# Optimization experiments

Measured on AMD Instinct MI355X. Metric: run time of the kernel, lower is better.

## Reference

```python
import jax, jax.numpy as jnp
import numpy as np

N = 4096      # tokens per modality
DIM = 514     # input feature dim
OUT = 256     # out_dim (per-head width, head=1)
NC = 2        # num_classes
LN_EPS = 1e-5


def setup_inputs() -> dict:
    key = jax.random.key(0)
    ks = jax.random.split(key, 12)
    def nrm(k, shape, s=0.02):
        return jax.random.normal(k, shape, dtype=jnp.float32) * s
    return {
        "t1": jax.random.normal(ks[0], (N, DIM), dtype=jnp.float32),
        "t2": jax.random.normal(ks[1], (N, DIM), dtype=jnp.float32),
        "t1c": jax.random.normal(ks[2], (N, DIM), dtype=jnp.float32),
        "Wqkv1": nrm(ks[3], (DIM, 3 * OUT)), "bqkv1": jnp.zeros((3 * OUT,), jnp.float32),
        "Wqkv2": nrm(ks[4], (DIM, 3 * OUT)), "bqkv2": jnp.zeros((3 * OUT,), jnp.float32),
        "Wqkv3": nrm(ks[5], (DIM, 3 * OUT)), "bqkv3": jnp.zeros((3 * OUT,), jnp.float32),
        "Wo1": nrm(ks[6], (2 * OUT, DIM)), "bo1": jnp.zeros((DIM,), jnp.float32),
        "Wo2": nrm(ks[7], (2 * OUT, DIM)), "bo2": jnp.zeros((DIM,), jnp.float32),
        "Wo3": nrm(ks[8], (2 * OUT, DIM)), "bo3": jnp.zeros((DIM,), jnp.float32),
        "ln_g": jnp.ones((3 * DIM,), jnp.float32),
        "ln_b": jnp.zeros((3 * DIM,), jnp.float32),
        "Wh": nrm(ks[9], (3 * DIM, NC)), "bh": jnp.zeros((NC,), jnp.float32),
    }


def _forward(t1, t2, t1c, Wqkv1, bqkv1, Wqkv2, bqkv2, Wqkv3, bqkv3,
             Wo1, bo1, Wo2, bo2, Wo3, bo3, ln_g, ln_b, Wh, bh):
    # QKV projections (head=1 so no head reshape needed)
    q1, k1, v1 = jnp.split(t1 @ Wqkv1 + bqkv1, 3, axis=-1)   # each [n, OUT]
    q2, k2, v2 = jnp.split(t2 @ Wqkv2 + bqkv2, 3, axis=-1)
    q3, k3, v3 = jnp.split(t1c @ Wqkv3 + bqkv3, 3, axis=-1)

    # Six cross-attention instances batched into one group dim g=6.
    # Order: out12, out13, out21, out23, out31, out32  (q_x attends to k_y/v_y)
    qs = jnp.stack([q2, q3, q1, q3, q1, q2])                  # [6, n, OUT]
    ks_ = jnp.stack([k1, k1, k2, k2, k3, k3])
    vs = jnp.stack([v1, v1, v2, v2, v3, v3])
    # NOTE: original code applies NO 1/sqrt(d) scale
    attn = jax.nn.softmax(jnp.einsum('gid,gjd->gij', qs, ks_), axis=-1)
    outs = jnp.einsum('gij,gjd->gid', attn, vs)               # [6, n, OUT]
    out12, out13, out21, out23, out31, out32 = outs

    # residual add with duplicated keys, then per-modality output proj + residual
    t1r = jnp.concatenate([out21, out31], -1) + jnp.concatenate([k1, k1], -1)
    t2r = jnp.concatenate([out12, out32], -1) + jnp.concatenate([k2, k2], -1)
    t3r = jnp.concatenate([out13, out23], -1) + jnp.concatenate([k3, k3], -1)
    a1 = t1r @ Wo1 + bo1 + t1                                 # [n, DIM]
    a2 = t2r @ Wo2 + bo2 + t2
    a3 = t3r @ Wo3 + bo3 + t1c

    atten = jnp.concatenate([a1, a2, a3], -1)                 # [n, 3*DIM]
    mu = jnp.mean(atten, axis=-1, keepdims=True)
    var = jnp.var(atten, axis=-1, keepdims=True)
    normed = (atten - mu) * jax.lax.rsqrt(var + LN_EPS) * ln_g + ln_b
    out = normed @ Wh + bh                                    # [n, NC]
    feat = atten[None]                                        # [1, n, 3*DIM]
    return out, feat


def reference(t1, t2, t1c, Wqkv1, bqkv1, Wqkv2, bqkv2, Wqkv3, bqkv3,
              Wo1, bo1, Wo2, bo2, Wo3, bo3, ln_g, ln_b, Wh, bh):
    return _forward(t1, t2, t1c, Wqkv1, bqkv1, Wqkv2, bqkv2, Wqkv3, bqkv3,
                    Wo1, bo1, Wo2, bo2, Wo3, bo3, ln_g, ln_b, Wh, bh)
```

## Files before the change

### kernel.cpp

```cpp
#include <hip/hip_runtime.h>
#include <hip/hip_bf16.h>

typedef unsigned short u16;
typedef unsigned int u32;
typedef __attribute__((ext_vector_type(8))) __bf16 bf16x8;
typedef __attribute__((ext_vector_type(4))) float f32x4;
typedef __attribute__((ext_vector_type(16))) float f32x16;

#define N_TOK 4096
#define DIMF  514
#define KPAD  544
#define OUT3  768
#define OUTD  256
#define RDIM  512
#define DIMP  640
#define FDIM  1542
#define SHIFT 16.0f
#define NCHUNK 4
#define KTILES ((N_TOK / NCHUNK) / 32)

__device__ __forceinline__ bf16x8 ld_frag(const u16* p) {
    return __builtin_bit_cast(bf16x8, *reinterpret_cast<const uint4*>(p));
}
__device__ __forceinline__ u16 f2bf(float x) {
    return __builtin_bit_cast(u16, __float2bfloat16(x));
}
__device__ __forceinline__ float bf2f(u16 u) {
    return __bfloat162float(__builtin_bit_cast(__hip_bfloat16, u));
}
__device__ __forceinline__ f32x16 mfma_b(bf16x8 a, bf16x8 b, f32x16 c) {
    return __builtin_amdgcn_mfma_f32_32x32x16_bf16(a, b, c, 0, 0, 0);
}
__device__ __forceinline__ f32x4 mfma16(bf16x8 a, bf16x8 b, f32x4 c) {
    return __builtin_amdgcn_mfma_f32_16x16x32_bf16(a, b, c, 0, 0, 0);
}
__device__ __forceinline__ void gl_lds16(const u16* g, u16* l) {
    __builtin_amdgcn_global_load_lds(
        (const __attribute__((address_space(1))) void*)(g),
        (__attribute__((address_space(3))) void*)(l), 16, 0, 0);
}

__global__ void prep_kernel(const float* __restrict__ t1, const float* __restrict__ t2,
                            const float* __restrict__ t1c,
                            const float* __restrict__ W1, const float* __restrict__ W2,
                            const float* __restrict__ W3,
                            const float* __restrict__ Wo1, const float* __restrict__ Wo2,
                            const float* __restrict__ Wo3,
                            u16* __restrict__ tA, u16* __restrict__ WqkvT,
                            u16* __restrict__ WoT)
{
    int idx = blockIdx.x * blockDim.x + threadIdx.x;
    const int TA_N = 3 * N_TOK * KPAD;
    const int WQ_N = 3 * OUT3 * KPAD;
    const int WO_N = 3 * DIMP * RDIM;
    if (idx < TA_N) {
        int m = idx / (N_TOK * KPAD);
        int rem = idx - m * (N_TOK * KPAD);
        int row = rem / KPAD;
        int col = rem - row * KPAD;
        const float* t = (m == 0) ? t1 : (m == 1) ? t2 : t1c;
        tA[idx] = (col < DIMF) ? f2bf(t[row * DIMF + col]) : (u16)0;
    } else if (idx < TA_N + WQ_N) {
        int i = idx - TA_N;
        int m = i / (OUT3 * KPAD);
        int rem = i - m * (OUT3 * KPAD);
        int n = rem / KPAD;
        int c = rem - n * KPAD;
        const float* W = (m == 0) ? W1 : (m == 1) ? W2 : W3;
        WqkvT[i] = (c < DIMF) ? f2bf(W[c * OUT3 + n]) : (u16)0;
    } else if (idx < TA_N + WQ_N + WO_N) {
        int i = idx - TA_N - WQ_N;
        int m = i / (DIMP * RDIM);
        int rem = i - m * (DIMP * RDIM);
        int n = rem / RDIM;
        int c = rem - n * RDIM;
        const float* W = (m == 0) ? Wo1 : (m == 1) ? Wo2 : Wo3;
        WoT[i] = (n < DIMF) ? f2bf(W[c * DIMF + n]) : (u16)0;
    }
}

__global__ __launch_bounds__(256, 2) void qkv_gemm(
    const u16* __restrict__ tA, const u16* __restrict__ WqkvT,
    const float* __restrict__ b1, const float* __restrict__ b2, const float* __restrict__ b3,
    u16* __restrict__ qbuf, u16* __restrict__ kbuf, u16* __restrict__ vT)
{
    const int mt = blockIdx.x, nt = blockIdx.y, mod = blockIdx.z;
    const u16* A = tA + mod * (N_TOK * KPAD);
    const u16* B = WqkvT + mod * (OUT3 * KPAD);
    const float* bias = (mod == 0) ? b1 : (mod == 1) ? b2 : b3;

    __shared__ alignas(16) u16 Fbuf[2][16 * 512];

    const int tid = threadIdx.x;
    const int lane = tid & 63;
    const int w = tid >> 6;
    const int wm = w & 1, wn = w >> 1;
    const int l31 = lane & 31, h = lane >> 5;

    auto stage = [&](int kt, u16* dst) {
#pragma unroll
        for (int fi = 0; fi < 4; fi++) {
            int f = w * 4 + fi;
            int rb = (f & 7) >> 1, kc = f & 1;
            const u16* src = (f < 8)
                ? &A[(mt * 128 + rb * 32 + l31) * KPAD + kt * 32 + kc * 16 + h * 8]
                : &B[(nt * 128 + rb * 32 + l31) * KPAD + kt * 32 + kc * 16 + h * 8];
            gl_lds16(src, dst + f * 512);
        }
    };

    f32x16 acc[2][2];
#pragma unroll
    for (int i = 0; i < 2; i++)
#pragma unroll
        for (int j = 0; j < 2; j++)
#pragma unroll
            for (int r = 0; r < 16; r++) acc[i][j][r] = 0.f;

    stage(0, Fbuf[0]);
    __syncthreads();

    for (int kt = 0; kt < KPAD / 32; kt++) {
        const int p = kt & 1;
        if (kt + 1 < KPAD / 32) stage(kt + 1, Fbuf[p ^ 1]);
        const u16* FB = Fbuf[p];
#pragma unroll
        for (int kc = 0; kc < 2; kc++) {
            bf16x8 af[2], bfr[2];
#pragma unroll
            for (int mr = 0; mr < 2; mr++)
                af[mr] = ld_frag(&FB[((wm * 2 + mr) * 2 + kc) * 512 + lane * 8]);
#pragma unroll
            for (int nr = 0; nr < 2; nr++)
                bfr[nr] = ld_frag(&FB[(8 + (wn * 2 + nr) * 2 + kc) * 512 + lane * 8]);
#pragma unroll
            for (int mr = 0; mr < 2; mr++)
#pragma unroll
                for (int nr = 0; nr < 2; nr++)
                    acc[mr][nr] = mfma_b(af[mr], bfr[nr], acc[mr][nr]);
        }
        __syncthreads();
    }

    u16* qb = qbuf + mod * (N_TOK * OUTD);
    u16* kb = kbuf + mod * (N_TOK * OUTD);
    u16* vb = vT + mod * (OUTD * N_TOK);
#pragma unroll
    for (int mr = 0; mr < 2; mr++)
#pragma unroll
        for (int nr = 0; nr < 2; nr++)
#pragma unroll
            for (int r = 0; r < 16; r++) {
                int row = mt * 128 + wm * 64 + mr * 32 + (r & 3) + 8 * (r >> 2) + 4 * h;
                int col = nt * 128 + wn * 64 + nr * 32 + l31;
                u16 bv = f2bf(acc[mr][nr][r] + bias[col]);
                int cs = col >> 8, cc = col & 255;
                if (cs == 0)      qb[row * OUTD + cc] = bv;
                else if (cs == 1) kb[row * OUTD + cc] = bv;
                else              vb[cc * N_TOK + row] = bv;
            }
}

__global__ __launch_bounds__(256, 2) void attn_kernel(
    const u16* __restrict__ qbuf, const u16* __restrict__ kbuf,
    const u16* __restrict__ vT, u16* __restrict__ Opart, float* __restrict__ lpart)
{
    const int qt = blockIdx.x;
    const int g  = blockIdx.y;
    const int c  = blockIdx.z;
    const int kv = g >> 1;
    const int mn = (kv == 0) ? 1 : 0;
    const int mx = (kv == 2) ? 1 : 2;
    const int qm = (g & 1) ? mx : mn;

    const u16* Qg = qbuf + qm * (N_TOK * OUTD);
    const u16* Kg = kbuf + kv * (N_TOK * OUTD);
    const u16* Vg = vT + kv * (OUTD * N_TOK);
    u16* Op = Opart + ((size_t)(c * 6 + g) * N_TOK + qt * 128) * OUTD;
    float* lp = lpart + (c * 6 + g) * N_TOK + qt * 128;

    __shared__ alignas(16) u16 Fbuf[2][32 * 512];

    const int tid = threadIdx.x;
    const int lane = tid & 63;
    const int w = tid >> 6;
    const int l31 = lane & 31, h = lane >> 5;
    const int sl = lane & 15, sg = lane >> 4;
    const int q0 = qt * 128 + w * 32;

    auto stage = [&](int k0, u16* dst) {
        if (w < 2) {
#pragma unroll
            for (int fi = 0; fi < 8; fi++) {
                gl_lds16(&Kg[(k0 + w * 16 + sl) * OUTD + fi * 32 + sg * 8],
                         dst + (w * 8 + fi) * 512);
            }
        } else {
#pragma unroll
            for (int fi = 0; fi < 8; fi++) {
                int f = (w - 2) * 8 + fi;
                int nb = f >> 1, half = f & 1;
                gl_lds16(&Vg[(nb * 32 + l31) * N_TOK + k0 + half * 16 + h * 8],
                         dst + (16 + f) * 512);
            }
        }
    };

    const int k0base = c * (N_TOK / NCHUNK);

    stage(k0base, Fbuf[0]);

    bf16x8 qf[16];
#pragma unroll
    for (int j = 0; j < 8; j++)
#pragma unroll
        for (int qh = 0; qh < 2; qh++)
            qf[2 * j + qh] = ld_frag(&Qg[(q0 + qh * 16 + sl) * OUTD + j * 32 + sg * 8]);

    f32x16 Oacc[8];
#pragma unroll
    for (int nb = 0; nb < 8; nb++)
#pragma unroll
        for (int r = 0; r < 16; r++) Oacc[nb][r] = 0.f;
    float lsA0 = 0.f, lsA1 = 0.f;

    __syncthreads();

    for (int kt = 0; kt < KTILES; kt++) {
        const int p = kt & 1;
        if (kt + 1 < KTILES) stage(k0base + (kt + 1) * 32, Fbuf[p ^ 1]);
        const u16* FB = Fbuf[p];

        f32x4 Sq[2][2];
#pragma unroll
        for (int a = 0; a < 2; a++)
#pragma unroll
            for (int b = 0; b < 2; b++)
#pragma unroll
                for (int r = 0; r < 4; r++) Sq[a][b][r] = 0.f;
        __builtin_amdgcn_s_setprio(1);
#pragma unroll
        for (int j = 0; j < 8; j++) {
            bf16x8 kf0 = ld_frag(&FB[j * 512 + lane * 8]);
            bf16x8 kf1 = ld_frag(&FB[(8 + j) * 512 + lane * 8]);
            Sq[0][0] = mfma16(kf0, qf[2 * j], Sq[0][0]);
            Sq[0][1] = mfma16(kf0, qf[2 * j + 1], Sq[0][1]);
            Sq[1][0] = mfma16(kf1, qf[2 * j], Sq[1][0]);
            Sq[1][1] = mfma16(kf1, qf[2 * j + 1], Sq[1][1]);
        }
        __builtin_amdgcn_s_setprio(0);

        u32 pk[2][2][2];
#pragma unroll
        for (int kh = 0; kh < 2; kh++)
#pragma unroll
            for (int qh = 0; qh < 2; qh++) {
                float e0 = __expf(Sq[kh][qh][0] - SHIFT);
                float e1 = __expf(Sq[kh][qh][1] - SHIFT);
                float e2 = __expf(Sq[kh][qh][2] - SHIFT);
                float e3 = __expf(Sq[kh][qh][3] - SHIFT);
                if (qh == 0) lsA0 += (e0 + e1) + (e2 + e3);
                else         lsA1 += (e0 + e1) + (e2 + e3);
                pk[qh][kh][0] = (u32)f2bf(e0) | ((u32)f2bf(e1) << 16);
                pk[qh][kh][1] = (u32)f2bf(e2) | ((u32)f2bf(e3) << 16);
            }

        asm volatile("v_permlane16_swap_b32 %0, %1" : "+v"(pk[0][0][0]), "+v"(pk[1][0][0]));
        asm volatile("v_permlane16_swap_b32 %0, %1" : "+v"(pk[0][0][1]), "+v"(pk[1][0][1]));
        asm volatile("v_permlane16_swap_b32 %0, %1" : "+v"(pk[0][1][0]), "+v"(pk[1][1][0]));
        asm volatile("v_permlane16_swap_b32 %0, %1" : "+v"(pk[0][1][1]), "+v"(pk[1][1][1]));
        uint4 b0, b1;
        b0.x = pk[0][0][0]; b0.y = pk[0][0][1]; b0.z = pk[1][0][0]; b0.w = pk[1][0][1];
        b1.x = pk[0][1][0]; b1.y = pk[0][1][1]; b1.z = pk[1][1][0]; b1.w = pk[1][1][1];
        bf16x8 pb0 = __builtin_bit_cast(bf16x8, b0);
        bf16x8 pb1 = __builtin_bit_cast(bf16x8, b1);

        __builtin_amdgcn_s_setprio(1);
#pragma unroll
        for (int nb = 0; nb < 8; nb++) {
            bf16x8 vf0 = ld_frag(&FB[(16 + 2 * nb) * 512 + lane * 8]);
            bf16x8 vf1 = ld_frag(&FB[(17 + 2 * nb) * 512 + lane * 8]);
            Oacc[nb] = mfma_b(vf0, pb0, Oacc[nb]);
            Oacc[nb] = mfma_b(vf1, pb1, Oacc[nb]);
        }
        __builtin_amdgcn_s_setprio(0);
        __syncthreads();
    }

    lsA0 += __shfl_xor(lsA0, 16, 64);
    lsA0 += __shfl_xor(lsA0, 32, 64);
    lsA1 += __shfl_xor(lsA1, 16, 64);
    lsA1 += __shfl_xor(lsA1, 32, 64);
    if (lane < 16)      lp[w * 32 + lane] = lsA0;
    else if (lane < 32) lp[w * 32 + lane] = lsA1;

    float* Tb = reinterpret_cast<float*>(&Fbuf[0][0]) + w * (32 * 33);
#pragma unroll
    for (int nb = 0; nb < 8; nb++) {
#pragma unroll
        for (int r = 0; r < 16; r++)
            Tb[((r & 3) + 8 * (r >> 2) + 4 * h) * 33 + l31] = Oacc[nb][r];
        __builtin_amdgcn_s_waitcnt(0);
#pragma unroll
        for (int qq = 0; qq < 16; qq++) {
            float v = Tb[l31 * 33 + qq * 2 + h];
            Op[(w * 32 + qq * 2 + h) * OUTD + nb * 32 + l31] = f2bf(v);
        }
        __builtin_amdgcn_s_waitcnt(0);
    }
}

__global__ __launch_bounds__(256, 1) void combine_kernel(
    const u16* __restrict__ Opart, const float* __restrict__ lpart,
    const u16* __restrict__ kbuf, u16* __restrict__ rbuf)
{
    const int q = blockIdx.x;
    const int g = blockIdx.y;
    const int d = threadIdx.x;
    const int kv = g >> 1;
    const int mn = (kv == 0) ? 1 : 0;
    const int mx = (kv == 2) ? 1 : 2;
    const int qm = (g & 1) ? mx : mn;
    const int sm = (qm == 0) ? 1 : 0;
    const int slot = (kv == sm) ? 0 : 1;

    float o = 0.f, l = 0.f;
#pragma unroll
    for (int c = 0; c < NCHUNK; c++) {
        o += bf2f(Opart[((size_t)(c * 6 + g) * N_TOK + q) * OUTD + d]);
        l += lpart[(c * 6 + g) * N_TOK + q];
    }
    float res = o / l + bf2f(kbuf[qm * (N_TOK * OUTD) + q * OUTD + d]);
    rbuf[qm * (size_t)(N_TOK * RDIM) + q * RDIM + slot * OUTD + d] = f2bf(res);
}

__global__ __launch_bounds__(256, 2) void proj_gemm(
    const u16* __restrict__ rbuf, const u16* __restrict__ WoT,
    const float* __restrict__ bo1, const float* __restrict__ bo2, const float* __restrict__ bo3,
    const float* __restrict__ t1, const float* __restrict__ t2, const float* __restrict__ t1c,
    float* __restrict__ feat)
{
    const int mt = blockIdx.x, nt = blockIdx.y, mod = blockIdx.z;
    const u16* A = rbuf + mod * (N_TOK * RDIM);
    const u16* B = WoT + mod * (DIMP * RDIM);
    const float* bias = (mod == 0) ? bo1 : (mod == 1) ? bo2 : bo3;
    const float* tres = (mod == 0) ? t1 : (mod == 1) ? t2 : t1c;

    __shared__ alignas(16) u16 Fbuf[2][16 * 512];

    const int tid = threadIdx.x;
    const int lane = tid & 63;
    const int w = tid >> 6;
    const int wm = w & 1, wn = w >> 1;
    const int l31 = lane & 31, h = lane >> 5;

    auto stage = [&](int kt, u16* dst) {
#pragma unroll
        for (int fi = 0; fi < 4; fi++) {
            int f = w * 4 + fi;
            int rb = (f & 7) >> 1, kc = f & 1;
            const u16* src = (f < 8)
                ? &A[(mt * 128 + rb * 32 + l31) * RDIM + kt * 32 + kc * 16 + h * 8]
                : &B[(nt * 128 + rb * 32 + l31) * RDIM + kt * 32 + kc * 16 + h * 8];
            gl_lds16(src, dst + f * 512);
        }
    };

    f32x16 acc[2][2];
#pragma unroll
    for (int i = 0; i < 2; i++)
#pragma unroll
        for (int j = 0; j < 2; j++)
#pragma unroll
            for (int r = 0; r < 16; r++) acc[i][j][r] = 0.f;

    stage(0, Fbuf[0]);
    __syncthreads();

    for (int kt = 0; kt < RDIM / 32; kt++) {
        const int p = kt & 1;
        if (kt + 1 < RDIM / 32) stage(kt + 1, Fbuf[p ^ 1]);
        const u16* FB = Fbuf[p];
#pragma unroll
        for (int kc = 0; kc < 2; kc++) {
            bf16x8 af[2], bfr[2];
#pragma unroll
            for (int mr = 0; mr < 2; mr++)
                af[mr] = ld_frag(&FB[((wm * 2 + mr) * 2 + kc) * 512 + lane * 8]);
#pragma unroll
            for (int nr = 0; nr < 2; nr++)
                bfr[nr] = ld_frag(&FB[(8 + (wn * 2 + nr) * 2 + kc) * 512 + lane * 8]);
#pragma unroll
            for (int mr = 0; mr < 2; mr++)
#pragma unroll
                for (int nr = 0; nr < 2; nr++)
                    acc[mr][nr] = mfma_b(af[mr], bfr[nr], acc[mr][nr]);
        }
        __syncthreads();
    }

#pragma unroll
    for (int mr = 0; mr < 2; mr++)
#pragma unroll
        for (int nr = 0; nr < 2; nr++)
#pragma unroll
            for (int r = 0; r < 16; r++) {
                int row = mt * 128 + wm * 64 + mr * 32 + (r & 3) + 8 * (r >> 2) + 4 * h;
                int col = nt * 128 + wn * 64 + nr * 32 + l31;
                if (col < DIMF) {
                    float v = acc[mr][nr][r] + bias[col] + tres[row * DIMF + col];
                    feat[row * FDIM + mod * DIMF + col] = v;
                }
            }
}

__global__ __launch_bounds__(256, 1) void ln_head(
    const float* __restrict__ feat, const float* __restrict__ gam,
    const float* __restrict__ bet, const float* __restrict__ Wh,
    const float* __restrict__ bh, float* __restrict__ out)
{
    const int row = blockIdx.x;
    const float* x = feat + row * FDIM;
    const int tid = threadIdx.x;
    float v[7];
    float s = 0.f, ss = 0.f;
#pragma unroll
    for (int i = 0; i < 7; i++) {
        int idx = tid + i * 256;
        float val = (idx < FDIM) ? x[idx] : 0.f;
        v[i] = val; s += val; ss += val * val;
    }
#pragma unroll
    for (int m = 1; m < 64; m <<= 1) { s += __shfl_xor(s, m, 64); ss += __shfl_xor(ss, m, 64); }
    __shared__ float red[8];
    const int w = tid >> 6, lane = tid & 63;
    if (lane == 0) { red[w] = s; red[4 + w] = ss; }
    __syncthreads();
    s = red[0] + red[1] + red[2] + red[3];
    ss = red[4] + red[5] + red[6] + red[7];
    const float mu = s / (float)FDIM;
    const float var = ss / (float)FDIM - mu * mu;
    const float rstd = rsqrtf(var + 1e-5f);
    float a0 = 0.f, a1 = 0.f;
#pragma unroll
    for (int i = 0; i < 7; i++) {
        int idx = tid + i * 256;
        if (idx < FDIM) {
            float nv = (v[i] - mu) * rstd * gam[idx] + bet[idx];
            a0 += nv * Wh[idx * 2];
            a1 += nv * Wh[idx * 2 + 1];
        }
    }
#pragma unroll
    for (int m = 1; m < 64; m <<= 1) { a0 += __shfl_xor(a0, m, 64); a1 += __shfl_xor(a1, m, 64); }
    __shared__ float red2[8];
    if (lane == 0) { red2[w] = a0; red2[4 + w] = a1; }
    __syncthreads();
    if (tid == 0) {
        out[row * 2 + 0] = red2[0] + red2[1] + red2[2] + red2[3] + bh[0];
        out[row * 2 + 1] = red2[4] + red2[5] + red2[6] + red2[7] + bh[1];
    }
}

extern "C" void kernel_launch(void* const* d_in, const int* in_sizes, int n_in,
                              void* d_out, int out_size, void* d_ws, size_t ws_size,
                              hipStream_t stream)
{
    const float* t1    = (const float*)d_in[0];
    const float* t2    = (const float*)d_in[1];
    const float* t1c   = (const float*)d_in[2];
    const float* Wqkv1 = (const float*)d_in[3];
    const float* bqkv1 = (const float*)d_in[4];
    const float* Wqkv2 = (const float*)d_in[5];
    const float* bqkv2 = (const float*)d_in[6];
    const float* Wqkv3 = (const float*)d_in[7];
    const float* bqkv3 = (const float*)d_in[8];
    const float* Wo1   = (const float*)d_in[9];
    const float* bo1   = (const float*)d_in[10];
    const float* Wo2   = (const float*)d_in[11];
    const float* bo2   = (const float*)d_in[12];
    const float* Wo3   = (const float*)d_in[13];
    const float* bo3   = (const float*)d_in[14];
    const float* ln_g  = (const float*)d_in[15];
    const float* ln_b  = (const float*)d_in[16];
    const float* Wh    = (const float*)d_in[17];
    const float* bh    = (const float*)d_in[18];

    char* ws = (char*)d_ws;
    size_t off = 0;
    u16* tA    = (u16*)(ws + off); off += (size_t)3 * N_TOK * KPAD * 2;
    u16* WqkvT = (u16*)(ws + off); off += (size_t)3 * OUT3 * KPAD * 2;
    u16* WoT   = (u16*)(ws + off); off += (size_t)3 * DIMP * RDIM * 2;
    u16* qbuf  = (u16*)(ws + off); off += (size_t)3 * N_TOK * OUTD * 2;
    u16* kbuf  = (u16*)(ws + off); off += (size_t)3 * N_TOK * OUTD * 2;
    u16* vT    = (u16*)(ws + off); off += (size_t)3 * OUTD * N_TOK * 2;
    u16* rbuf  = (u16*)(ws + off); off += (size_t)3 * N_TOK * RDIM * 2;
    u16* Opart = (u16*)(ws + off); off += (size_t)NCHUNK * 6 * N_TOK * OUTD * 2;
    float* lpart = (float*)(ws + off); off += (size_t)NCHUNK * 6 * N_TOK * 4;

    float* out  = (float*)d_out;
    float* feat = out + N_TOK * 2;

    const int prep_total = 3 * N_TOK * KPAD + 3 * OUT3 * KPAD + 3 * DIMP * RDIM;
    prep_kernel<<<(prep_total + 255) / 256, 256, 0, stream>>>(
        t1, t2, t1c, Wqkv1, Wqkv2, Wqkv3, Wo1, Wo2, Wo3, tA, WqkvT, WoT);

    qkv_gemm<<<dim3(32, 6, 3), 256, 0, stream>>>(
        tA, WqkvT, bqkv1, bqkv2, bqkv3, qbuf, kbuf, vT);

    attn_kernel<<<dim3(32, 6, NCHUNK), 256, 0, stream>>>(qbuf, kbuf, vT, Opart, lpart);

    combine_kernel<<<dim3(N_TOK, 6), 256, 0, stream>>>(Opart, lpart, kbuf, rbuf);

    proj_gemm<<<dim3(32, 5, 3), 256, 0, stream>>>(
        rbuf, WoT, bo1, bo2, bo3, t1, t2, t1c, feat);

    ln_head<<<4096, 256, 0, stream>>>(feat, ln_g, ln_b, Wh, bh, out);
}
```

Before: 330.7 us.

## Widen attention blocks to 512 threads with triple-buffered K/V staging

The attention kernel now uses 8 waves per block covering 256 query rows, so each staged K/V tile is shared by twice as many queries, and the grid is halved. The LDS ring grows from two to three tiles in dynamic shared memory, with prefetch two tiles ahead. The full __syncthreads is replaced by a partial vmcnt wait plus barrier so the newest prefetch can stay in flight. This aims to cut global K/V traffic per query and hide load latency, at the cost of 96KB LDS per block and fewer blocks, which may limit occupancy.

```diff
diff --git a/kernel.cpp b/kernel.cpp
--- a/kernel.cpp
+++ b/kernel.cpp
@@ -18,6 +18,8 @@
 #define SHIFT 16.0f
 #define NCHUNK 4
 #define KTILES ((N_TOK / NCHUNK) / 32)
+#define TILE_U16 (32 * 512)
+#define ATTN_LDS (3 * TILE_U16 * 2)
 
 __device__ __forceinline__ bf16x8 ld_frag(const u16* p) {
     return __builtin_bit_cast(bf16x8, *reinterpret_cast<const uint4*>(p));
@@ -161,7 +163,7 @@
             }
 }
 
-__global__ __launch_bounds__(256, 2) void attn_kernel(
+__global__ __launch_bounds__(512, 2) void attn_kernel(
     const u16* __restrict__ qbuf, const u16* __restrict__ kbuf,
     const u16* __restrict__ vT, u16* __restrict__ Opart, float* __restrict__ lpart)
 {
@@ -176,39 +178,39 @@
     const u16* Qg = qbuf + qm * (N_TOK * OUTD);
     const u16* Kg = kbuf + kv * (N_TOK * OUTD);
     const u16* Vg = vT + kv * (OUTD * N_TOK);
-    u16* Op = Opart + ((size_t)(c * 6 + g) * N_TOK + qt * 128) * OUTD;
-    float* lp = lpart + (c * 6 + g) * N_TOK + qt * 128;
-
-    __shared__ alignas(16) u16 Fbuf[2][32 * 512];
+    u16* Op = Opart + ((size_t)(c * 6 + g) * N_TOK + qt * 256) * OUTD;
+    float* lp = lpart + (c * 6 + g) * N_TOK + qt * 256;
+
+    extern __shared__ u16 Fdyn[];
 
     const int tid = threadIdx.x;
     const int lane = tid & 63;
     const int w = tid >> 6;
     const int l31 = lane & 31, h = lane >> 5;
     const int sl = lane & 15, sg = lane >> 4;
-    const int q0 = qt * 128 + w * 32;
+    const int q0 = qt * 256 + w * 32;
 
     auto stage = [&](int k0, u16* dst) {
-        if (w < 2) {
-#pragma unroll
-            for (int fi = 0; fi < 8; fi++) {
-                gl_lds16(&Kg[(k0 + w * 16 + sl) * OUTD + fi * 32 + sg * 8],
-                         dst + (w * 8 + fi) * 512);
+        if (w < 4) {
+#pragma unroll
+            for (int fi = 0; fi < 4; fi++) {
+                int f = w * 4 + fi;
+                int kh = f >> 3, j = f & 7;
+                gl_lds16(&Kg[(k0 + kh * 16 + sl) * OUTD + j * 32 + sg * 8],
+                         dst + f * 512);
             }
         } else {
 #pragma unroll
-            for (int fi = 0; fi < 8; fi++) {
-                int f = (w - 2) * 8 + fi;
-                int nb = f >> 1, half = f & 1;
+            for (int fi = 0; fi < 4; fi++) {
+                int fv = (w - 4) * 4 + fi;
+                int nb = fv >> 1, half = fv & 1;
                 gl_lds16(&Vg[(nb * 32 + l31) * N_TOK + k0 + half * 16 + h * 8],
-                         dst + (16 + f) * 512);
+                         dst + (16 + fv) * 512);
             }
         }
     };
 
     const int k0base = c * (N_TOK / NCHUNK);
-
-    stage(k0base, Fbuf[0]);
 
     bf16x8 qf[16];
 #pragma unroll
@@ -217,6 +219,9 @@
         for (int qh = 0; qh < 2; qh++)
             qf[2 * j + qh] = ld_frag(&Qg[(q0 + qh * 16 + sl) * OUTD + j * 32 + sg * 8]);
 
+    stage(k0base, Fdyn);
+    stage(k0base + 32, Fdyn + TILE_U16);
+
     f32x16 Oacc[8];
 #pragma unroll
     for (int nb = 0; nb < 8; nb++)
@@ -224,12 +229,16 @@
         for (int r = 0; r < 16; r++) Oacc[nb][r] = 0.f;
     float lsA0 = 0.f, lsA1 = 0.f;
 
-    __syncthreads();
+    asm volatile("s_waitcnt vmcnt(0)" ::: "memory");
+    __builtin_amdgcn_s_barrier();
+
+    u16* Bc = Fdyn;
+    u16* Bn = Fdyn + TILE_U16;
+    u16* Bp = Fdyn + 2 * TILE_U16;
 
     for (int kt = 0; kt < KTILES; kt++) {
-        const int p = kt & 1;
-        if (kt + 1 < KTILES) stage(k0base + (kt + 1) * 32, Fbuf[p ^ 1]);
-        const u16* FB = Fbuf[p];
+        if (kt + 2 < KTILES) stage(k0base + (kt + 2) * 32, Bp);
+        const u16* FB = Bc;
 
         f32x4 Sq[2][2];
 #pragma unroll
@@ -284,7 +293,11 @@
             Oacc[nb] = mfma_b(vf1, pb1, Oacc[nb]);
         }
         __builtin_amdgcn_s_setprio(0);
-        __syncthreads();
+
+        asm volatile("s_waitcnt vmcnt(4)" ::: "memory");
+        __builtin_amdgcn_s_barrier();
+
+        u16* t = Bc; Bc = Bn; Bn = Bp; Bp = t;
     }
 
     lsA0 += __shfl_xor(lsA0, 16, 64);
@@ -294,7 +307,7 @@
     if (lane < 16)      lp[w * 32 + lane] = lsA0;
     else if (lane < 32) lp[w * 32 + lane] = lsA1;
 
-    float* Tb = reinterpret_cast<float*>(&Fbuf[0][0]) + w * (32 * 33);
+    float* Tb = reinterpret_cast<float*>(Fdyn) + w * (32 * 33);
 #pragma unroll
     for (int nb = 0; nb < 8; nb++) {
 #pragma unroll
@@ -501,6 +514,9 @@
     float* out  = (float*)d_out;
     float* feat = out + N_TOK * 2;
 
+    hipFuncSetAttribute(reinterpret_cast<const void*>(attn_kernel),
+                        hipFuncAttributeMaxDynamicSharedMemorySize, ATTN_LDS);
+
     const int prep_total = 3 * N_TOK * KPAD + 3 * OUT3 * KPAD + 3 * DIMP * RDIM;
     prep_kernel<<<(prep_total + 255) / 256, 256, 0, stream>>>(
         t1, t2, t1c, Wqkv1, Wqkv2, Wqkv3, Wo1, Wo2, Wo3, tA, WqkvT, WoT);
@@ -508,7 +524,8 @@
     qkv_gemm<<<dim3(32, 6, 3), 256, 0, stream>>>(
         tA, WqkvT, bqkv1, bqkv2, bqkv3, qbuf, kbuf, vT);
 
-    attn_kernel<<<dim3(32, 6, NCHUNK), 256, 0, stream>>>(qbuf, kbuf, vT, Opart, lpart);
+    attn_kernel<<<dim3(16, 6, NCHUNK), 512, ATTN_LDS, stream>>>(
+        qbuf, kbuf, vT, Opart, lpart);
 
     combine_kernel<<<dim3(N_TOK, 6), 256, 0, stream>>>(Opart, lpart, kbuf, rbuf);
 
```

New measurement: 339.1 us. +2.6%, slower.

## Retile attention to 16-query waves with 16-key tiles and fewer KV chunks

Applied to the files above, without the earlier changes.

Restructures the attention kernel so each wave owns 16 queries and each iteration processes a 16-key tile. The P·V product now uses the 16x16x16 bf16 MFMA with 16 output blocks, which removes the permlane swap shuffling. The grid changes to 64 query tiles with 2 KV chunks, and occupancy is requested at 3 blocks per CU. In exchange, each K/V tile is reused by half as many queries, barriers come twice as often per key, and the k16 MFMA variant may have lower throughput than the k32 form it replaces.

```diff
diff --git a/kernel.cpp b/kernel.cpp
--- a/kernel.cpp
+++ b/kernel.cpp
@@ -4,6 +4,8 @@
 typedef unsigned short u16;
 typedef unsigned int u32;
 typedef __attribute__((ext_vector_type(8))) __bf16 bf16x8;
+typedef __attribute__((ext_vector_type(4))) __bf16 bf16x4;
+typedef __attribute__((ext_vector_type(4))) short short4v;
 typedef __attribute__((ext_vector_type(4))) float f32x4;
 typedef __attribute__((ext_vector_type(16))) float f32x16;
 
@@ -16,8 +18,9 @@
 #define DIMP  640
 #define FDIM  1542
 #define SHIFT 16.0f
-#define NCHUNK 4
-#define KTILES ((N_TOK / NCHUNK) / 32)
+#define NCHUNK 2
+#define KTILES ((N_TOK / NCHUNK) / 16)
+#define TILE_U16 8192
 
 __device__ __forceinline__ bf16x8 ld_frag(const u16* p) {
     return __builtin_bit_cast(bf16x8, *reinterpret_cast<const uint4*>(p));
@@ -33,6 +36,18 @@
 }
 __device__ __forceinline__ f32x4 mfma16(bf16x8 a, bf16x8 b, f32x4 c) {
     return __builtin_amdgcn_mfma_f32_16x16x32_bf16(a, b, c, 0, 0, 0);
+}
+__device__ __forceinline__ f32x4 mfma16k16(bf16x4 a, bf16x4 b, f32x4 c) {
+#if __has_builtin(__builtin_amdgcn_mfma_f32_16x16x16_bf16)
+    return __builtin_amdgcn_mfma_f32_16x16x16_bf16(a, b, c, 0, 0, 0);
+#elif __has_builtin(__builtin_amdgcn_mfma_f32_16x16x16bf16_1k)
+    return __builtin_amdgcn_mfma_f32_16x16x16bf16_1k(
+        __builtin_bit_cast(short4v, a), __builtin_bit_cast(short4v, b), c, 0, 0, 0);
+#else
+    asm volatile("v_mfma_f32_16x16x16_bf16 %0, %1, %2, %0"
+                 : "+v"(c) : "v"(a), "v"(b));
+    return c;
+#endif
 }
 __device__ __forceinline__ void gl_lds16(const u16* g, u16* l) {
     __builtin_amdgcn_global_load_lds(
@@ -161,7 +176,7 @@
             }
 }
 
-__global__ __launch_bounds__(256, 2) void attn_kernel(
+__global__ __launch_bounds__(256, 3) void attn_kernel(
     const u16* __restrict__ qbuf, const u16* __restrict__ kbuf,
     const u16* __restrict__ vT, u16* __restrict__ Opart, float* __restrict__ lpart)
 {
@@ -176,32 +191,31 @@
     const u16* Qg = qbuf + qm * (N_TOK * OUTD);
     const u16* Kg = kbuf + kv * (N_TOK * OUTD);
     const u16* Vg = vT + kv * (OUTD * N_TOK);
-    u16* Op = Opart + ((size_t)(c * 6 + g) * N_TOK + qt * 128) * OUTD;
-    float* lp = lpart + (c * 6 + g) * N_TOK + qt * 128;
-
-    __shared__ alignas(16) u16 Fbuf[2][32 * 512];
+    u16* Op = Opart + ((size_t)(c * 6 + g) * N_TOK + qt * 64) * OUTD;
+    float* lp = lpart + (c * 6 + g) * N_TOK + qt * 64;
+
+    __shared__ alignas(16) u16 Fbuf[2][TILE_U16];
 
     const int tid = threadIdx.x;
     const int lane = tid & 63;
     const int w = tid >> 6;
+    const int sl = lane & 15, sg = lane >> 4;
     const int l31 = lane & 31, h = lane >> 5;
-    const int sl = lane & 15, sg = lane >> 4;
-    const int q0 = qt * 128 + w * 32;
+    const int q0 = qt * 64 + w * 16;
 
     auto stage = [&](int k0, u16* dst) {
         if (w < 2) {
 #pragma unroll
-            for (int fi = 0; fi < 8; fi++) {
-                gl_lds16(&Kg[(k0 + w * 16 + sl) * OUTD + fi * 32 + sg * 8],
-                         dst + (w * 8 + fi) * 512);
+            for (int fi = 0; fi < 4; fi++) {
+                int j = w * 4 + fi;
+                gl_lds16(&Kg[(k0 + sl) * OUTD + j * 32 + sg * 8], dst + j * 512);
             }
         } else {
 #pragma unroll
-            for (int fi = 0; fi < 8; fi++) {
-                int f = (w - 2) * 8 + fi;
-                int nb = f >> 1, half = f & 1;
-                gl_lds16(&Vg[(nb * 32 + l31) * N_TOK + k0 + half * 16 + h * 8],
-                         dst + (16 + f) * 512);
+            for (int fi = 0; fi < 4; fi++) {
+                int sv = (w - 2) * 4 + fi;
+                gl_lds16(&Vg[(sv * 32 + l31) * N_TOK + k0 + h * 8],
+                         dst + (8 + sv) * 512);
             }
         }
     };
@@ -210,102 +224,81 @@
 
     stage(k0base, Fbuf[0]);
 
-    bf16x8 qf[16];
+    bf16x8 qf[8];
 #pragma unroll
     for (int j = 0; j < 8; j++)
-#pragma unroll
-        for (int qh = 0; qh < 2; qh++)
-            qf[2 * j + qh] = ld_frag(&Qg[(q0 + qh * 16 + sl) * OUTD + j * 32 + sg * 8]);
-
-    f32x16 Oacc[8];
-#pragma unroll
-    for (int nb = 0; nb < 8; nb++)
-#pragma unroll
-        for (int r = 0; r < 16; r++) Oacc[nb][r] = 0.f;
-    float lsA0 = 0.f, lsA1 = 0.f;
+        qf[j] = ld_frag(&Qg[(q0 + sl) * OUTD + j * 32 + sg * 8]);
+
+    f32x4 Oacc[16];
+#pragma unroll
+    for (int nb = 0; nb < 16; nb++)
+#pragma unroll
+        for (int r = 0; r < 4; r++) Oacc[nb][r] = 0.f;
+    float lsum = 0.f;
 
     __syncthreads();
 
     for (int kt = 0; kt < KTILES; kt++) {
         const int p = kt & 1;
-        if (kt + 1 < KTILES) stage(k0base + (kt + 1) * 32, Fbuf[p ^ 1]);
+        if (kt + 1 < KTILES) stage(k0base + (kt + 1) * 16, Fbuf[p ^ 1]);
         const u16* FB = Fbuf[p];
 
-        f32x4 Sq[2][2];
-#pragma unroll
-        for (int a = 0; a < 2; a++)
-#pragma unroll
-            for (int b = 0; b < 2; b++)
-#pragma unroll
-                for (int r = 0; r < 4; r++) Sq[a][b][r] = 0.f;
+        f32x4 Sa, Sb;
+#pragma unroll
+        for (int r = 0; r < 4; r++) { Sa[r] = 0.f; Sb[r] = 0.f; }
         __builtin_amdgcn_s_setprio(1);
 #pragma unroll
-        for (int j = 0; j < 8; j++) {
-            bf16x8 kf0 = ld_frag(&FB[j * 512 + lane * 8]);
-            bf16x8 kf1 = ld_frag(&FB[(8 + j) * 512 + lane * 8]);
-            Sq[0][0] = mfma16(kf0, qf[2 * j], Sq[0][0]);
-            Sq[0][1] = mfma16(kf0, qf[2 * j + 1], Sq[0][1]);
-            Sq[1][0] = mfma16(kf1, qf[2 * j], Sq[1][0]);
-            Sq[1][1] = mfma16(kf1, qf[2 * j + 1], Sq[1][1]);
+        for (int j = 0; j < 4; j++) {
+            bf16x8 kfa = ld_frag(&FB[j * 512 + lane * 8]);
+            bf16x8 kfb = ld_frag(&FB[(4 + j) * 512 + lane * 8]);
+            Sa = mfma16(kfa, qf[j], Sa);
+            Sb = mfma16(kfb, qf[4 + j], Sb);
         }
         __builtin_amdgcn_s_setprio(0);
 
-        u32 pk[2][2][2];
-#pragma unroll
-        for (int kh = 0; kh < 2; kh++)
-#pragma unroll
-            for (int qh = 0; qh < 2; qh++) {
-                float e0 = __expf(Sq[kh][qh][0] - SHIFT);
-                float e1 = __expf(Sq[kh][qh][1] - SHIFT);
-                float e2 = __expf(Sq[kh][qh][2] - SHIFT);
-                float e3 = __expf(Sq[kh][qh][3] - SHIFT);
-                if (qh == 0) lsA0 += (e0 + e1) + (e2 + e3);
-                else         lsA1 += (e0 + e1) + (e2 + e3);
-                pk[qh][kh][0] = (u32)f2bf(e0) | ((u32)f2bf(e1) << 16);
-                pk[qh][kh][1] = (u32)f2bf(e2) | ((u32)f2bf(e3) << 16);
-            }
-
-        asm volatile("v_permlane16_swap_b32 %0, %1" : "+v"(pk[0][0][0]), "+v"(pk[1][0][0]));
-        asm volatile("v_permlane16_swap_b32 %0, %1" : "+v"(pk[0][0][1]), "+v"(pk[1][0][1]));
-        asm volatile("v_permlane16_swap_b32 %0, %1" : "+v"(pk[0][1][0]), "+v"(pk[1][1][0]));
-        asm volatile("v_permlane16_swap_b32 %0, %1" : "+v"(pk[0][1][1]), "+v"(pk[1][1][1]));
-        uint4 b0, b1;
-        b0.x = pk[0][0][0]; b0.y = pk[0][0][1]; b0.z = pk[1][0][0]; b0.w = pk[1][0][1];
-        b1.x = pk[0][1][0]; b1.y = pk[0][1][1]; b1.z = pk[1][1][0]; b1.w = pk[1][1][1];
-        bf16x8 pb0 = __builtin_bit_cast(bf16x8, b0);
-        bf16x8 pb1 = __builtin_bit_cast(bf16x8, b1);
+        float e0 = __expf(Sa[0] + Sb[0] - SHIFT);
+        float e1 = __expf(Sa[1] + Sb[1] - SHIFT);
+        float e2 = __expf(Sa[2] + Sb[2] - SHIFT);
+        float e3 = __expf(Sa[3] + Sb[3] - SHIFT);
+        lsum += (e0 + e1) + (e2 + e3);
+        uint2 pbu;
+        pbu.x = (u32)f2bf(e0) | ((u32)f2bf(e1) << 16);
+        pbu.y = (u32)f2bf(e2) | ((u32)f2bf(e3) << 16);
+        bf16x4 pb = __builtin_bit_cast(bf16x4, pbu);
 
         __builtin_amdgcn_s_setprio(1);
 #pragma unroll
-        for (int nb = 0; nb < 8; nb++) {
-            bf16x8 vf0 = ld_frag(&FB[(16 + 2 * nb) * 512 + lane * 8]);
-            bf16x8 vf1 = ld_frag(&FB[(17 + 2 * nb) * 512 + lane * 8]);
-            Oacc[nb] = mfma_b(vf0, pb0, Oacc[nb]);
-            Oacc[nb] = mfma_b(vf1, pb1, Oacc[nb]);
+        for (int nb = 0; nb < 16; nb++) {
+            int voff = (8 + (nb >> 1)) * 512
+                     + ((nb & 1) * 16 + sl + 32 * (sg >> 1)) * 8 + (sg & 1) * 4;
+            bf16x4 vf = __builtin_bit_cast(bf16x4,
+                *reinterpret_cast<const uint2*>(&FB[voff]));
+            Oacc[nb] = mfma16k16(vf, pb, Oacc[nb]);
         }
         __builtin_amdgcn_s_setprio(0);
         __syncthreads();
     }
 
-    lsA0 += __shfl_xor(lsA0, 16, 64);
-    lsA0 += __shfl_xor(lsA0, 32, 64);
-    lsA1 += __shfl_xor(lsA1, 16, 64);
-    lsA1 += __shfl_xor(lsA1, 32, 64);
-    if (lane < 16)      lp[w * 32 + lane] = lsA0;
-    else if (lane < 32) lp[w * 32 + lane] = lsA1;
-
-    float* Tb = reinterpret_cast<float*>(&Fbuf[0][0]) + w * (32 * 33);
-#pragma unroll
-    for (int nb = 0; nb < 8; nb++) {
-#pragma unroll
-        for (int r = 0; r < 16; r++)
-            Tb[((r & 3) + 8 * (r >> 2) + 4 * h) * 33 + l31] = Oacc[nb][r];
+    lsum += __shfl_xor(lsum, 16, 64);
+    lsum += __shfl_xor(lsum, 32, 64);
+    if (lane < 16) lp[w * 16 + lane] = lsum;
+
+    float* Tb = reinterpret_cast<float*>(&Fbuf[0][0]) + w * (16 * 17);
+#pragma unroll
+    for (int nb = 0; nb < 16; nb++) {
+#pragma unroll
+        for (int r = 0; r < 4; r++)
+            Tb[(sg * 4 + r) * 17 + sl] = Oacc[nb][r];
         __builtin_amdgcn_s_waitcnt(0);
-#pragma unroll
-        for (int qq = 0; qq < 16; qq++) {
-            float v = Tb[l31 * 33 + qq * 2 + h];
-            Op[(w * 32 + qq * 2 + h) * OUTD + nb * 32 + l31] = f2bf(v);
-        }
+        int qq = lane >> 2, d4 = (lane & 3) * 4;
+        float v0 = Tb[(d4 + 0) * 17 + qq];
+        float v1 = Tb[(d4 + 1) * 17 + qq];
+        float v2 = Tb[(d4 + 2) * 17 + qq];
+        float v3 = Tb[(d4 + 3) * 17 + qq];
+        uint2 sv;
+        sv.x = (u32)f2bf(v0) | ((u32)f2bf(v1) << 16);
+        sv.y = (u32)f2bf(v2) | ((u32)f2bf(v3) << 16);
+        *reinterpret_cast<uint2*>(&Op[(w * 16 + qq) * OUTD + nb * 16 + d4]) = sv;
         __builtin_amdgcn_s_waitcnt(0);
     }
 }
@@ -508,7 +501,7 @@
     qkv_gemm<<<dim3(32, 6, 3), 256, 0, stream>>>(
         tA, WqkvT, bqkv1, bqkv2, bqkv3, qbuf, kbuf, vT);
 
-    attn_kernel<<<dim3(32, 6, NCHUNK), 256, 0, stream>>>(qbuf, kbuf, vT, Opart, lpart);
+    attn_kernel<<<dim3(64, 6, NCHUNK), 256, 0, stream>>>(qbuf, kbuf, vT, Opart, lpart);
 
     combine_kernel<<<dim3(N_TOK, 6), 256, 0, stream>>>(Opart, lpart, kbuf, rbuf);
 
```

New measurement: 402.8 us. 21.8% more time.
